# Performance work log

Measured on AMD Instinct MI355X. Metric: run time of the kernel, lower is better.

The kernel has to match this reference:

```python
import jax, jax.numpy as jnp
import numpy as np

B, S, E = 2, 2048, 1024
H = 16
D = E // H  # 64
SCALE = D ** -0.5


def setup_inputs() -> dict:
    key = jax.random.key(0)
    ks = jax.random.split(key, 9)
    w = lambda k: jax.random.normal(k, (E, E), dtype=jnp.float32) * 0.02
    b = lambda k: jax.random.normal(k, (E,), dtype=jnp.float32) * 0.02
    return {
        "hidden_states": jax.random.normal(ks[0], (B, S, E), dtype=jnp.float32),
        "q_w": w(ks[1]), "q_b": b(ks[2]),
        "k_w": w(ks[3]), "k_b": b(ks[4]),
        "v_w": w(ks[5]), "v_b": b(ks[6]),
        "o_w": w(ks[7]), "o_b": b(ks[8]),
    }


def reference(hidden_states, q_w, q_b, k_w, k_b, v_w, v_b, o_w, o_b):
    dtype = hidden_states.dtype
    # torch Linear: y = x @ W^T + b
    q = hidden_states @ q_w.T + q_b
    k = hidden_states @ k_w.T + k_b
    v = hidden_states @ v_w.T + v_b
    # [B,S,E] -> [B*H, S, D]
    split = lambda t: t.reshape(B, S, H, D).transpose(0, 2, 1, 3).reshape(B * H, S, D)
    q, k, v = split(q), split(k), split(v)
    # upcast_attention: fp32 QK^T, scaled (baddbmm with beta=0, no mask)
    scores = SCALE * jnp.einsum("bqd,bkd->bqk", q.astype(jnp.float32), k.astype(jnp.float32))
    # upcast_softmax: fp32 softmax over last dim (transpose_qk=False), cast back
    probs = jax.nn.softmax(scores, axis=-1).astype(dtype)
    # PV bmm, merge heads, out_proj (dropout p=0.0 -> identity)
    out = jnp.einsum("bqk,bkd->bqd", probs, v)
    out = out.reshape(B, H, S, D).transpose(0, 2, 1, 3).reshape(B, S, E)
    return out @ o_w.T + o_b
```

## Files before the change

### kernel.cpp

```cpp
#include <hip/hip_runtime.h>

typedef __bf16 bf16x8 __attribute__((ext_vector_type(8)));
typedef __bf16 bf16x4 __attribute__((ext_vector_type(4)));
typedef float  f32x4  __attribute__((ext_vector_type(4)));
typedef float  f32x16 __attribute__((ext_vector_type(16)));
typedef unsigned int u32x4 __attribute__((ext_vector_type(4)));

#define CS 0.18033688011112042f

__device__ __forceinline__ float fast_exp2(float x) {
    return __builtin_amdgcn_exp2f(x);
}

__device__ __forceinline__ void gload_lds16(const __bf16* g, __bf16* l) {
    __builtin_amdgcn_global_load_lds(
        (const __attribute__((address_space(1))) void*)g,
        (__attribute__((address_space(3))) void*)l, 16, 0, 0);
}

__device__ __forceinline__ f32x4 MFMA(bf16x8 a, bf16x8 b, f32x4 c) {
    return __builtin_amdgcn_mfma_f32_16x16x32_bf16(a, b, c, 0, 0, 0);
}
__device__ __forceinline__ f32x16 MFMA32(bf16x8 a, bf16x8 b, f32x16 c) {
    return __builtin_amdgcn_mfma_f32_32x32x16_bf16(a, b, c, 0, 0, 0);
}

__device__ __forceinline__ unsigned pk2(float a, float b) {
    union { __bf16 h[2]; unsigned u; } x;
    x.h[0] = (__bf16)a; x.h[1] = (__bf16)b;
    return x.u;
}

__device__ __forceinline__ void swap32(unsigned &a, unsigned &b) {
    asm volatile("v_permlane32_swap_b32 %0, %1" : "+v"(a), "+v"(b));
}

__global__ __launch_bounds__(256) void cvt5_kernel(
    const float* __restrict__ s0, const float* __restrict__ s1,
    const float* __restrict__ s2, const float* __restrict__ s3,
    const float* __restrict__ s4,
    __bf16* __restrict__ d0, __bf16* __restrict__ d1, __bf16* __restrict__ d2,
    __bf16* __restrict__ d3, __bf16* __restrict__ d4)
{
    int blk = blockIdx.x;
    const float* src; __bf16* dst; int base;
    if (blk < 4096)      { src = s0; dst = d0; base = blk; }
    else if (blk < 5120) { src = s1; dst = d1; base = blk - 4096; }
    else if (blk < 6144) { src = s2; dst = d2; base = blk - 5120; }
    else if (blk < 7168) { src = s3; dst = d3; base = blk - 6144; }
    else                 { src = s4; dst = d4; base = blk - 7168; }
    int i = base * 1024 + threadIdx.x * 4;
    float4 v = *(const float4*)(src + i);
    bf16x4 o;
    o[0] = (__bf16)v.x; o[1] = (__bf16)v.y; o[2] = (__bf16)v.z; o[3] = (__bf16)v.w;
    *(bf16x4*)(dst + i) = o;
}

template <typename OutT, int BN>
__device__ __forceinline__ void gemm_core(const __bf16* __restrict__ A,
                                          const __bf16* __restrict__ W,
                                          const float* __restrict__ bias,
                                          OutT* __restrict__ C,
                                          int m0, int n0, bool vtrans, float oscale)
{
    constexpr int NJ  = BN / 32;
    constexpr int BCH = BN / 32;
    __shared__ __bf16 As[128 * 64];
    __shared__ __bf16 Bs[BN * 64];

    const int tid  = threadIdx.x;
    const int lane = tid & 63;
    const int w    = tid >> 6;
    const int wm   = w & 1;
    const int wn   = w >> 1;
    const int s    = lane & 15;
    const int q    = lane >> 4;

    const int srow = lane >> 3;
    const int scol = (lane & 7) ^ srow;

    f32x4 acc[4][NJ];
#pragma unroll
    for (int i = 0; i < 4; i++)
#pragma unroll
        for (int j = 0; j < NJ; j++)
#pragma unroll
            for (int r = 0; r < 4; r++) acc[i][j][r] = 0.0f;

    for (int k0 = 0; k0 < 1024; k0 += 64) {
        __syncthreads();
#pragma unroll
        for (int t = 0; t < 4; t++) {
            int chunk = w * 4 + t;
            int row   = chunk * 8 + srow;
            gload_lds16(A + (size_t)(m0 + row) * 1024 + k0 + scol * 8,
                        &As[chunk * 512]);
        }
#pragma unroll
        for (int t = 0; t < BCH; t++) {
            int chunk = w * BCH + t;
            int row   = chunk * 8 + srow;
            gload_lds16(W + (size_t)(n0 + row) * 1024 + k0 + scol * 8,
                        &Bs[chunk * 512]);
        }
        __syncthreads();

#pragma unroll
        for (int kk = 0; kk < 2; kk++) {
            bf16x8 af[4], bf[NJ];
#pragma unroll
            for (int i = 0; i < 4; i++) {
                int row = wm * 64 + i * 16 + s;
                af[i] = *(const bf16x8*)&As[row * 64 + ((((kk << 2) + q) ^ (row & 7)) << 3)];
            }
#pragma unroll
            for (int j = 0; j < NJ; j++) {
                int row = wn * (BN / 2) + j * 16 + s;
                bf[j] = *(const bf16x8*)&Bs[row * 64 + ((((kk << 2) + q) ^ (row & 7)) << 3)];
            }
#pragma unroll
            for (int i = 0; i < 4; i++)
#pragma unroll
                for (int j = 0; j < NJ; j++)
                    acc[i][j] = MFMA(af[i], bf[j], acc[i][j]);
        }
    }

    if (vtrans) {
        __bf16* Vt = (__bf16*)C;
#pragma unroll
        for (int j = 0; j < NJ; j++) {
            int col = n0 + wn * (BN / 2) + j * 16 + s;
            int h   = col >> 6;
            int d   = col & 63;
            float bv = bias[col];
#pragma unroll
            for (int i = 0; i < 4; i++) {
                int rowb = m0 + wm * 64 + i * 16 + q * 4;
                int b    = rowb >> 11;
                int sr   = rowb & 2047;
                bf16x4 pk;
#pragma unroll
                for (int r = 0; r < 4; r++) pk[r] = (__bf16)(acc[i][j][r] + bv);
                *(bf16x4*)&Vt[(size_t)((b * 16 + h) * 64 + d) * 2048 + sr] = pk;
            }
        }
    } else {
#pragma unroll
        for (int j = 0; j < NJ; j++) {
            int col = n0 + wn * (BN / 2) + j * 16 + s;
            float bv = bias[col];
#pragma unroll
            for (int i = 0; i < 4; i++) {
                int rowb = m0 + wm * 64 + i * 16 + q * 4;
#pragma unroll
                for (int r = 0; r < 4; r++) {
                    C[(size_t)(rowb + r) * 1024 + col] = (OutT)((acc[i][j][r] + bv) * oscale);
                }
            }
        }
    }
}

__global__ __launch_bounds__(256) void gemm_qkv_kernel(
    const __bf16* __restrict__ X,
    const __bf16* __restrict__ Wq, const float* __restrict__ bq,
    const __bf16* __restrict__ Wk, const float* __restrict__ bk,
    const __bf16* __restrict__ Wv, const float* __restrict__ bv,
    __bf16* __restrict__ Q, __bf16* __restrict__ K, __bf16* __restrict__ Vt)
{
    int mt   = blockIdx.x & 31;
    int ntot = blockIdx.x >> 5;
    int which = ntot >> 3;
    const __bf16* W    = (which == 0) ? Wq : (which == 1) ? Wk : Wv;
    const float*  bias = (which == 0) ? bq : (which == 1) ? bk : bv;
    __bf16*       Out  = (which == 0) ? Q  : (which == 1) ? K  : Vt;
    float oscale = (which == 0) ? CS : 1.0f;
    gemm_core<__bf16, 128>(X, W, bias, Out, mt * 128, (ntot & 7) * 128, which == 2, oscale);
}

__global__ __launch_bounds__(256) void gemm_o_kernel(
    const __bf16* __restrict__ Ain, const __bf16* __restrict__ Wo,
    const float* __restrict__ bo, float* __restrict__ Out)
{
    int mt = blockIdx.x & 31;
    int nt = blockIdx.x >> 5;
    gemm_core<float, 64>(Ain, Wo, bo, Out, mt * 128, nt * 64, false, 1.0f);
}

__global__ __launch_bounds__(512, 4) void attn_kernel(
    const __bf16* __restrict__ Q, const __bf16* __restrict__ K,
    const __bf16* __restrict__ Vt, __bf16* __restrict__ O)
{
    __shared__ __bf16 smem[2][2][2][64 * 64];

    const int bh = blockIdx.x >> 4;
    const int qt = blockIdx.x & 15;
    const int b  = bh >> 4;
    const int h  = bh & 15;

    const int tid  = threadIdx.x;
    const int lane = tid & 63;
    const int w    = tid >> 6;
    const int g    = w >> 2;
    const int ws   = w & 3;
    const int gv   = w & 3;
    const int qc   = lane & 31;
    const int hi   = lane >> 5;

    const int lr8 = lane >> 3;
    const int pcb = lane & 7;

    bf16x8 bq[4];
    {
        const int qrow = qt * 128 + ws * 32 + qc;
        const __bf16* qp = Q + (size_t)(b * 2048 + qrow) * 1024 + h * 64 + hi * 8;
#pragma unroll
        for (int kd = 0; kd < 4; kd++)
            bq[kd] = *(const bf16x8*)(qp + kd * 16);
    }

    const f32x16 fzero = 0.0f;
    f32x16 acc[2];
#pragma unroll
    for (int nb = 0; nb < 2; nb++) acc[nb] = fzero;
    float lst = 0.0f;

    const __bf16* Kbase = K  + (size_t)(b * 2048 + g * 1024) * 1024 + h * 64;
    const __bf16* Vbase = Vt + (size_t)bh * 64 * 2048 + g * 1024;

    auto stage = [&](int bf, int kb) {
        __bf16* kdst = smem[g][bf][0];
        __bf16* vdst = smem[g][bf][1];
#pragma unroll
        for (int t = 0; t < 2; t++) {
            int sc  = gv * 2 + t;
            int r   = sc * 8 + lr8;
            int lcb = pcb ^ (r & 7);
            gload_lds16(Kbase + (size_t)(kb + r) * 1024 + lcb * 8,
                        kdst + sc * 512);
            gload_lds16(Vbase + (size_t)r * 2048 + kb + lcb * 8,
                        vdst + sc * 512);
        }
    };

    stage(0, 0);
    __syncthreads();

    int cur = 0;
    for (int kc = 0; kc < 16; kc++) {
        stage(cur ^ 1, ((kc + 1) & 15) * 64);

        const __bf16* kbuf = smem[g][cur][0];
        const __bf16* vbuf = smem[g][cur][1];

        f32x16 sc[2];
#pragma unroll
        for (int mb = 0; mb < 2; mb++) {
            int row = mb * 32 + qc;
            int rsw = row & 7;
            bf16x8 af0 = *(const bf16x8*)&kbuf[row * 64 + ((hi ^ rsw) << 3)];
            __builtin_amdgcn_s_setprio(1);
            sc[mb] = MFMA32(af0, bq[0], fzero);
            __builtin_amdgcn_s_setprio(0);
#pragma unroll
            for (int kd = 1; kd < 4; kd++) {
                bf16x8 af = *(const bf16x8*)&kbuf[row * 64 + ((((kd << 1) | hi) ^ rsw) << 3)];
                __builtin_amdgcn_s_setprio(1);
                sc[mb] = MFMA32(af, bq[kd], sc[mb]);
                __builtin_amdgcn_s_setprio(0);
            }
        }

#pragma unroll
        for (int mb = 0; mb < 2; mb++) {
            float e[16];
#pragma unroll
            for (int r = 0; r < 16; r++)
                e[r] = fast_exp2(sc[mb][r]);
            float s0 = 0.f, s1 = 0.f, s2 = 0.f, s3 = 0.f;
#pragma unroll
            for (int r = 0; r < 16; r += 4) {
                s0 += e[r]; s1 += e[r + 1]; s2 += e[r + 2]; s3 += e[r + 3];
            }
            lst += (s0 + s1) + (s2 + s3);
#pragma unroll
            for (int bb = 0; bb < 2; bb++) {
                unsigned w0 = pk2(e[8 * bb + 0], e[8 * bb + 1]);
                unsigned w1 = pk2(e[8 * bb + 2], e[8 * bb + 3]);
                unsigned w2 = pk2(e[8 * bb + 4], e[8 * bb + 5]);
                unsigned w3 = pk2(e[8 * bb + 6], e[8 * bb + 7]);
                swap32(w0, w2);
                swap32(w1, w3);
                u32x4 pw; pw[0] = w0; pw[1] = w1; pw[2] = w2; pw[3] = w3;
                bf16x8 pa = __builtin_bit_cast(bf16x8, pw);
                int kslot = ((mb << 1) | bb) << 1;
                bf16x8 bv0 = *(const bf16x8*)&vbuf[(0 * 32 + qc) * 64 + (((kslot | hi) ^ (qc & 7)) << 3)];
                bf16x8 bv1 = *(const bf16x8*)&vbuf[(1 * 32 + qc) * 64 + (((kslot | hi) ^ ((32 + qc) & 7)) << 3)];
                __builtin_amdgcn_s_setprio(1);
                acc[0] = MFMA32(pa, bv0, acc[0]);
                acc[1] = MFMA32(pa, bv1, acc[1]);
                __builtin_amdgcn_s_setprio(0);
            }
        }
        __syncthreads();
        cur ^= 1;
    }

    float* cbuf = (float*)&smem[0][0][0][0];
    if (g == 1) {
        float* p = cbuf + ((size_t)ws * 64 + lane) * 36;
        *(f32x16*)(p)      = acc[0];
        *(f32x16*)(p + 16) = acc[1];
        p[32] = lst;
    }
    __syncthreads();
    if (g == 0) {
        float* p = cbuf + ((size_t)ws * 64 + lane) * 36;
        acc[0] += *(const f32x16*)(p);
        acc[1] += *(const f32x16*)(p + 16);
        lst += p[32];

        float lt2 = lst + __shfl_xor(lst, 32);

        const size_t obase = (size_t)(b * 2048 + qt * 128 + ws * 32) * 1024 + h * 64;
#pragma unroll
        for (int r = 0; r < 16; r++) {
            int row_rel = (r & 3) + 8 * (r >> 2) + 4 * hi;
            float lr = __shfl(lt2, row_rel);
            float inv = 1.0f / lr;
#pragma unroll
            for (int nb = 0; nb < 2; nb++) {
                O[obase + (size_t)row_rel * 1024 + nb * 32 + qc] = (__bf16)(acc[nb][r] * inv);
            }
        }
    }
}

extern "C" void kernel_launch(void* const* d_in, const int* in_sizes, int n_in,
                              void* d_out, int out_size, void* d_ws, size_t ws_size,
                              hipStream_t stream)
{
    const float* hs = (const float*)d_in[0];
    const float* qw = (const float*)d_in[1];
    const float* qb = (const float*)d_in[2];
    const float* kw = (const float*)d_in[3];
    const float* kb = (const float*)d_in[4];
    const float* vw = (const float*)d_in[5];
    const float* vb = (const float*)d_in[6];
    const float* ow = (const float*)d_in[7];
    const float* ob = (const float*)d_in[8];
    float* out = (float*)d_out;

    char* ws = (char*)d_ws;
    const size_t MB = (size_t)1024 * 1024;
    __bf16* Xb  = (__bf16*)(ws);
    __bf16* Wqb = (__bf16*)(ws +  8 * MB);
    __bf16* Wkb = (__bf16*)(ws + 10 * MB);
    __bf16* Wvb = (__bf16*)(ws + 12 * MB);
    __bf16* Wob = (__bf16*)(ws + 14 * MB);
    __bf16* Qb  = (__bf16*)(ws + 16 * MB);
    __bf16* Kb  = (__bf16*)(ws + 24 * MB);
    __bf16* Vtb = (__bf16*)(ws + 32 * MB);
    __bf16* Ab  = (__bf16*)(ws + 40 * MB);

    cvt5_kernel<<<dim3(8192), dim3(256), 0, stream>>>(hs, qw, kw, vw, ow,
                                                      Xb, Wqb, Wkb, Wvb, Wob);

    gemm_qkv_kernel<<<dim3(768), dim3(256), 0, stream>>>(Xb, Wqb, qb, Wkb, kb, Wvb, vb,
                                                         Qb, Kb, Vtb);
    attn_kernel<<<dim3(512), dim3(512), 0, stream>>>(Qb, Kb, Vtb, Ab);
    gemm_o_kernel<<<dim3(512), dim3(256), 0, stream>>>(Ab, Wob, ob, out);
}
```

Before: 195.2 us.

## Software-pipeline attention loop: overlap QK^T of next tile with PV of previous

Restructures the attention inner loop so that each iteration computes QK^T and the softmax/pack for key tile k while running the PV MFMAs for tile k-1. The packed probabilities are carried across iterations in registers. V gets a triple-buffered LDS ring and K stays double-buffered, so a V tile is kept until its deferred PV step has run. The goal is to hide the exp/pack latency behind independent MFMA work and drop the redundant wraparound prefetch of the final iteration. In exchange LDS use per block rises from 64KB to 80KB, register pressure from the carried operands goes up, and there is extra prologue and epilogue code.

```diff
diff --git a/kernel.cpp b/kernel.cpp
--- a/kernel.cpp
+++ b/kernel.cpp
@@ -192,7 +192,7 @@
     const __bf16* __restrict__ Q, const __bf16* __restrict__ K,
     const __bf16* __restrict__ Vt, __bf16* __restrict__ O)
 {
-    __shared__ __bf16 smem[2][2][2][64 * 64];
+    __shared__ __bf16 smem[16384 + 24576];
 
     const int bh = blockIdx.x >> 4;
     const int qt = blockIdx.x & 15;
@@ -208,6 +208,9 @@
     const int qc   = lane & 31;
     const int hi   = lane >> 5;
 
+    __bf16* kt = smem + g * 2 * 4096;
+    __bf16* vt = smem + 16384 + g * 3 * 4096;
+
     const int lr8 = lane >> 3;
     const int pcb = lane & 7;
 
@@ -229,55 +232,53 @@
     const __bf16* Kbase = K  + (size_t)(b * 2048 + g * 1024) * 1024 + h * 64;
     const __bf16* Vbase = Vt + (size_t)bh * 64 * 2048 + g * 1024;
 
-    auto stage = [&](int bf, int kb) {
-        __bf16* kdst = smem[g][bf][0];
-        __bf16* vdst = smem[g][bf][1];
+    auto stage_k = [&](int bf, int kb) {
 #pragma unroll
         for (int t = 0; t < 2; t++) {
-            int sc  = gv * 2 + t;
-            int r   = sc * 8 + lr8;
+            int sc8 = gv * 2 + t;
+            int r   = sc8 * 8 + lr8;
             int lcb = pcb ^ (r & 7);
             gload_lds16(Kbase + (size_t)(kb + r) * 1024 + lcb * 8,
-                        kdst + sc * 512);
+                        kt + bf * 4096 + sc8 * 512);
+        }
+    };
+    auto stage_v = [&](int bf, int kb) {
+#pragma unroll
+        for (int t = 0; t < 2; t++) {
+            int sc8 = gv * 2 + t;
+            int r   = sc8 * 8 + lr8;
+            int lcb = pcb ^ (r & 7);
             gload_lds16(Vbase + (size_t)r * 2048 + kb + lcb * 8,
-                        vdst + sc * 512);
+                        vt + bf * 4096 + sc8 * 512);
         }
     };
 
-    stage(0, 0);
-    __syncthreads();
-
-    int cur = 0;
-    for (int kc = 0; kc < 16; kc++) {
-        stage(cur ^ 1, ((kc + 1) & 15) * 64);
-
-        const __bf16* kbuf = smem[g][cur][0];
-        const __bf16* vbuf = smem[g][cur][1];
-
-        f32x16 sc[2];
+    auto qkt = [&](const __bf16* kbuf, f32x16* sc2) {
 #pragma unroll
         for (int mb = 0; mb < 2; mb++) {
             int row = mb * 32 + qc;
             int rsw = row & 7;
             bf16x8 af0 = *(const bf16x8*)&kbuf[row * 64 + ((hi ^ rsw) << 3)];
             __builtin_amdgcn_s_setprio(1);
-            sc[mb] = MFMA32(af0, bq[0], fzero);
+            sc2[mb] = MFMA32(af0, bq[0], fzero);
             __builtin_amdgcn_s_setprio(0);
 #pragma unroll
             for (int kd = 1; kd < 4; kd++) {
                 bf16x8 af = *(const bf16x8*)&kbuf[row * 64 + ((((kd << 1) | hi) ^ rsw) << 3)];
                 __builtin_amdgcn_s_setprio(1);
-                sc[mb] = MFMA32(af, bq[kd], sc[mb]);
+                sc2[mb] = MFMA32(af, bq[kd], sc2[mb]);
                 __builtin_amdgcn_s_setprio(0);
             }
         }
-
+    };
+
+    auto sm_pack = [&](const f32x16* sc2, bf16x8* pa) {
 #pragma unroll
         for (int mb = 0; mb < 2; mb++) {
             float e[16];
 #pragma unroll
             for (int r = 0; r < 16; r++)
-                e[r] = fast_exp2(sc[mb][r]);
+                e[r] = fast_exp2(sc2[mb][r]);
             float s0 = 0.f, s1 = 0.f, s2 = 0.f, s3 = 0.f;
 #pragma unroll
             for (int r = 0; r < 16; r += 4) {
@@ -293,21 +294,54 @@
                 swap32(w0, w2);
                 swap32(w1, w3);
                 u32x4 pw; pw[0] = w0; pw[1] = w1; pw[2] = w2; pw[3] = w3;
-                bf16x8 pa = __builtin_bit_cast(bf16x8, pw);
-                int kslot = ((mb << 1) | bb) << 1;
-                bf16x8 bv0 = *(const bf16x8*)&vbuf[(0 * 32 + qc) * 64 + (((kslot | hi) ^ (qc & 7)) << 3)];
-                bf16x8 bv1 = *(const bf16x8*)&vbuf[(1 * 32 + qc) * 64 + (((kslot | hi) ^ ((32 + qc) & 7)) << 3)];
-                __builtin_amdgcn_s_setprio(1);
-                acc[0] = MFMA32(pa, bv0, acc[0]);
-                acc[1] = MFMA32(pa, bv1, acc[1]);
-                __builtin_amdgcn_s_setprio(0);
-            }
-        }
+                pa[(mb << 1) | bb] = __builtin_bit_cast(bf16x8, pw);
+            }
+        }
+    };
+
+    auto pv = [&](const bf16x8* pa, const __bf16* vbuf) {
+#pragma unroll
+        for (int pk = 0; pk < 4; pk++) {
+            int kslot = pk << 1;
+            bf16x8 bv0 = *(const bf16x8*)&vbuf[qc * 64        + (((kslot | hi) ^ (qc & 7)) << 3)];
+            bf16x8 bv1 = *(const bf16x8*)&vbuf[(32 + qc) * 64 + (((kslot | hi) ^ (qc & 7)) << 3)];
+            __builtin_amdgcn_s_setprio(1);
+            acc[0] = MFMA32(pa[pk], bv0, acc[0]);
+            acc[1] = MFMA32(pa[pk], bv1, acc[1]);
+            __builtin_amdgcn_s_setprio(0);
+        }
+    };
+
+    stage_k(0, 0); stage_v(0, 0);
+    __syncthreads();
+    stage_k(1, 64); stage_v(1, 64);
+
+    bf16x8 pa[4];
+    {
+        f32x16 sc2[2];
+        qkt(kt, sc2);
+        sm_pack(sc2, pa);
+    }
+    __syncthreads();
+
+    int kbi = 1, vprev = 0, vstage = 2;
+    int kb = 128;
+    for (int kc = 1; kc < 16; kc++) {
+        if (kc < 15) { stage_k(kbi ^ 1, kb); stage_v(vstage, kb); }
+        f32x16 sc2[2];
+        qkt(kt + kbi * 4096, sc2);
+        pv(pa, vt + vprev * 4096);
+        sm_pack(sc2, pa);
         __syncthreads();
-        cur ^= 1;
-    }
-
-    float* cbuf = (float*)&smem[0][0][0][0];
+        kbi ^= 1;
+        vprev  = (vprev  == 2) ? 0 : vprev + 1;
+        vstage = (vstage == 2) ? 0 : vstage + 1;
+        kb += 64;
+    }
+    pv(pa, vt);
+
+    __syncthreads();
+    float* cbuf = (float*)smem;
     if (g == 1) {
         float* p = cbuf + ((size_t)ws * 64 + lane) * 36;
         *(f32x16*)(p)      = acc[0];
```

Result: slower. 202.8 us (+3.9%).
